# Kernel optimization log

Hardware: AMD Instinct MI355X
Metric: run time of the kernel (lower is better)

## Reference

```python
import jax, jax.numpy as jnp
import numpy as np

NB, C, N, H, W = 2, 128, 4, 64, 64
K = 9  # 3x3 kernel positions


def _conv(x, w, b, pad):
    y = jax.lax.conv_general_dilated(x, w, (1, 1), ((pad, pad), (pad, pad)),
                                     dimension_numbers=('NCHW', 'OIHW', 'NCHW'))
    return y + b[None, :, None, None]


def _bn(x, g, be, m, v, eps=1e-5):
    scale = g / jnp.sqrt(v + eps)
    return x * scale[None, :, None, None] + (be - m * scale)[None, :, None, None]


def _maxpool(x):
    # MaxPool2d(kernel_size=2, stride=1, padding=1): output H+1, W+1
    return jax.lax.reduce_window(x, -jnp.inf, jax.lax.max, (1, 1, 2, 2), (1, 1, 1, 1),
                                 ((0, 0), (0, 0), (1, 1), (1, 1)))


def _deform_conv(x, offset, mask, w, b):
    # modulated deformable conv v2, kernel 3x3, stride 1, padding 1
    n, c, h, wd = x.shape
    ky = jnp.repeat(jnp.arange(3), 3).astype(x.dtype)  # kernel row offsets
    kx = jnp.tile(jnp.arange(3), 3).astype(x.dtype)    # kernel col offsets
    dy = offset[:, 0::2]  # [n,K,h,w] (torchvision layout: interleaved dy,dx)
    dx = offset[:, 1::2]
    py = jnp.arange(h, dtype=x.dtype)[None, None, :, None] - 1.0 + ky[None, :, None, None] + dy
    px = jnp.arange(wd, dtype=x.dtype)[None, None, None, :] - 1.0 + kx[None, :, None, None] + dx
    y0 = jnp.floor(py)
    x0 = jnp.floor(px)
    wy = py - y0
    wx = px - x0
    xt = jnp.transpose(x, (0, 2, 3, 1))  # [n,h,w,c]
    bidx = jnp.arange(n)[:, None, None, None]

    def gather(yi, xi):
        valid = ((yi >= 0) & (yi < h) & (xi >= 0) & (xi < wd)).astype(x.dtype)
        yc = jnp.clip(yi, 0, h - 1).astype(jnp.int32)
        xc = jnp.clip(xi, 0, wd - 1).astype(jnp.int32)
        return xt[bidx, yc, xc] * valid[..., None]  # [n,K,h,w,c]

    v = (((1 - wy) * (1 - wx))[..., None] * gather(y0, x0)
         + ((1 - wy) * wx)[..., None] * gather(y0, x0 + 1)
         + (wy * (1 - wx))[..., None] * gather(y0 + 1, x0)
         + (wy * wx)[..., None] * gather(y0 + 1, x0 + 1))
    v = v * mask[..., None]  # modulation mask [n,K,h,w]
    out = jnp.einsum('nkhwc,ock->nohw', v, w.reshape(w.shape[0], c, K))
    return out + b[None, :, None, None]


def _forward(x, w1, b1, g1, be1, m1, v1, w_off, b_off, w_mod, b_mod, w_def, b_def,
             g2, be2, m2, v2, w_ds, b_ds, g3, be3, m3, v3):
    for i in range(NB):
        h = jax.nn.relu(_bn(_conv(x, w1[i], b1[i], 1), g1[i], be1[i], m1[i], v1[i]))
        off = _conv(h, w_off[i], b_off[i], 1)
        msk = 2.0 * jax.nn.sigmoid(_conv(h, w_mod[i], b_mod[i], 1))
        d = _bn(_deform_conv(h, off, msk, w_def[i], b_def[i]), g2[i], be2[i], m2[i], v2[i])
        res = _bn(_conv(x, w_ds[i], b_ds[i], 0), g3[i], be3[i], m3[i], v3[i])
        x = _maxpool(jax.nn.relu(d + res))
    return x


def setup_inputs() -> dict:
    key = jax.random.key(0)
    ks = iter(jax.random.split(key, 48))

    def rn(shape, s=0.05):
        return jax.random.normal(next(ks), shape, jnp.float32) * s

    def bnp():
        g = jax.random.uniform(next(ks), (NB, C), jnp.float32) * 0.5 + 0.75
        be = rn((NB, C), 0.1)
        m = rn((NB, C), 0.1)
        v = jax.random.uniform(next(ks), (NB, C), jnp.float32) * 0.5 + 0.75
        return g, be, m, v

    g1, be1, m1, v1 = bnp()
    g2, be2, m2, v2 = bnp()
    g3, be3, m3, v3 = bnp()
    return dict(
        x=jax.random.normal(next(ks), (N, C, H, W), jnp.float32),
        w1=rn((NB, C, C, 3, 3)), b1=rn((NB, C)),
        g1=g1, be1=be1, m1=m1, v1=v1,
        w_off=rn((NB, 2 * K, C, 3, 3), 0.01), b_off=rn((NB, 2 * K), 0.01),
        w_mod=rn((NB, K, C, 3, 3), 0.01), b_mod=rn((NB, K), 0.01),
        w_def=rn((NB, C, C, 3, 3)), b_def=rn((NB, C)),
        g2=g2, be2=be2, m2=m2, v2=v2,
        w_ds=rn((NB, C, C, 1, 1)), b_ds=rn((NB, C)),
        g3=g3, be3=be3, m3=m3, v3=v3,
    )


def reference(x, w1, b1, g1, be1, m1, v1, w_off, b_off, w_mod, b_mod, w_def, b_def,
              g2, be2, m2, v2, w_ds, b_ds, g3, be3, m3, v3):
    return _forward(x, w1, b1, g1, be1, m1, v1, w_off, b_off, w_mod, b_mod, w_def, b_def,
                    g2, be2, m2, v2, w_ds, b_ds, g3, be3, m3, v3)
```

## Files before the change

kernel.cpp:

```cpp
#include <hip/hip_runtime.h>
#include <math.h>

constexpr int NN = 4;
constexpr int CC = 128;

typedef unsigned short u16;
typedef short bfrag __attribute__((ext_vector_type(8)));
typedef float facc  __attribute__((ext_vector_type(4)));

__device__ __forceinline__ float bf2f(u16 v) {
    unsigned u = ((unsigned)v) << 16; float f; __builtin_memcpy(&f, &u, 4); return f;
}
__device__ __forceinline__ u16 f2bf(float f) {
    unsigned u; __builtin_memcpy(&u, &f, 4);
    unsigned r = u + 0x7FFFu + ((u >> 16) & 1u);
    return (u16)(r >> 16);
}

typedef const __attribute__((address_space(1))) unsigned int gu32;
typedef __attribute__((address_space(3))) unsigned int lu32;
__device__ __forceinline__ void gload16(const u16* g, u16* l) {
    __builtin_amdgcn_global_load_lds((gu32*)g, (lu32*)l, 16, 0, 0);
}

template<int WM, int WN, int MR, int NR, int NOB, int EPI>
__global__ __launch_bounds__(512)
void gconv_h(const u16* __restrict__ A, const u16* __restrict__ Wp,
             const float* __restrict__ bias, void* __restrict__ Out,
             int H, int W, int npb)
{
    constexpr int HALOW = 68;
    __shared__ __align__(16) u16 halo[4 * HALOW * 128];

    const int Hp = H + 2, Wq = W + 2, HW = H * W;
    const int tid = threadIdx.x, lane = tid & 63, wv = tid >> 6;
    const int wn = wv % WN, wm = wv / WN;
    const int colc = lane & 15, kg = lane >> 4;
    const int n = blockIdx.x / npb;
    const int pib = (blockIdx.x - n * npb) * 64;
    const int ymin = pib / W;

    {
        const u16* Abase = A + (size_t)n * Hp * Wq * 128;
        for (int c = wv; c < 4 * HALOW / 4; c += 8) {
            int o = c * 512 + lane * 8;
            int r = o / (HALOW * 128);
            int e = o - r * (HALOW * 128);
            int x = e >> 7;
            int g = (e >> 3) & 15;
            int xs = x < Wq ? x : Wq - 1;
            int pr = ymin + r; if (pr > Hp - 1) pr = Hp - 1;
            const u16* src = Abase + ((size_t)pr * Wq + xs) * 128 + (g ^ (x & 7)) * 8;
            gload16(src, &halo[c * 512]);
        }
    }
    __syncthreads();

    int dyr[MR], axr[MR];
#pragma unroll
    for (int r = 0; r < MR; ++r) {
        int m = wm * (MR * 16) + r * 16 + colc;
        int pixl = pib + m; if (pixl > HW - 1) pixl = HW - 1;
        int y = pixl / W;
        dyr[r] = y - ymin; axr[r] = pixl - y * W;
    }

    auto wfrag = [&](int tap, int cc, int q) -> const bfrag* {
        return (const bfrag*)(Wp + (size_t)tap * (NOB * 2048)
                              + ((cc * NOB + wn * NR + q) * 64 + lane) * 8);
    };

    bfrag bc[4][NR];
#pragma unroll
    for (int cc = 0; cc < 4; ++cc)
#pragma unroll
        for (int q = 0; q < NR; ++q) bc[cc][q] = *wfrag(0, cc, q);

    facc acc[MR][NR];
#pragma unroll
    for (int r = 0; r < MR; ++r)
#pragma unroll
        for (int q = 0; q < NR; ++q) acc[r][q] = (facc){0.f, 0.f, 0.f, 0.f};

#pragma unroll 1
    for (int t = 0; t < 9; ++t) {
        int ty = t / 3, tx = t - ty * 3;
        bfrag bn_[4][NR];
        if (t < 8) {
#pragma unroll
            for (int cc = 0; cc < 4; ++cc)
#pragma unroll
                for (int q = 0; q < NR; ++q) bn_[cc][q] = *wfrag(t + 1, cc, q);
        }
#pragma unroll
        for (int cc = 0; cc < 4; ++cc) {
            bfrag a[MR];
#pragma unroll
            for (int r = 0; r < MR; ++r) {
                int xx = axr[r] + tx;
                a[r] = *(const bfrag*)&halo[((dyr[r] + ty) * HALOW + xx) * 128
                                            + ((cc * 4 + kg) ^ (xx & 7)) * 8];
            }
#pragma unroll
            for (int r = 0; r < MR; ++r)
#pragma unroll
                for (int q = 0; q < NR; ++q)
                    acc[r][q] = __builtin_amdgcn_mfma_f32_16x16x32_bf16(a[r], bc[cc][q], acc[r][q], 0, 0, 0);
        }
        if (t < 8) {
#pragma unroll
            for (int cc = 0; cc < 4; ++cc)
#pragma unroll
                for (int q = 0; q < NR; ++q) bc[cc][q] = bn_[cc][q];
        }
    }

#pragma unroll
    for (int r = 0; r < MR; ++r) {
#pragma unroll
        for (int j = 0; j < 4; ++j) {
            int m = wm * (MR * 16) + r * 16 + kg * 4 + j;
            int pixl = pib + m;
            if (pixl >= HW) continue;
#pragma unroll
            for (int q = 0; q < NR; ++q) {
                int oc = wn * (NR * 16) + q * 16 + colc;
                float val = acc[r][q][j] + bias[oc];
                if constexpr (EPI == 0) {
                    val = fmaxf(val, 0.f);
                    int y = pixl / W, x = pixl - y * W;
                    ((u16*)Out)[((size_t)(n * Hp + y + 1) * Wq + x + 1) * 128 + oc] = f2bf(val);
                } else {
                    if (oc >= 18) val = 2.f / (1.f + expf(-val));
                    ((float*)Out)[((size_t)n * HW + pixl) * 32 + oc] = val;
                }
            }
        }
    }
}

__global__ __launch_bounds__(512, 4)
void deform2_k(const u16* __restrict__ Hb, const u16* __restrict__ Xp,
               const float* __restrict__ OM, const u16* __restrict__ Wp,
               const float* __restrict__ biasC, float* __restrict__ T,
               int H, int W, int tw, int th)
{
    __shared__ __align__(16) u16 halo[96 * 16 * 8];
    __shared__ __align__(16) float oml[32 * 32];
    __shared__ __align__(16) u16 As2[2][32 * 128];

    const int Hp = H + 2, Wq = W + 2, HW = H * W;
    const int tid = threadIdx.x, lane = tid & 63, wv = tid >> 6;
    const int wn = wv & 3, wm = wv >> 2;
    const int colc = lane & 15, kg = lane >> 4;
    int bt = blockIdx.x;
    int n = bt / (tw * th); int rt = bt - n * (tw * th);
    int ty0 = (rt / tw) * 4, tx0 = (rt - (rt / tw) * tw) * 8;
    const u16* Hbase = Hb + (size_t)n * Hp * Wq * 128;

#pragma unroll
    for (int c = 0; c < 3; ++c) {
        int g = c * 512 + tid;
        int s = g >> 4, u = g & 15;
        int row = s / 12, col = s - row * 12;
        int gy = min(max(ty0 - 2 + row, 0), H - 1);
        int gx = min(max(tx0 - 2 + col, 0), W - 1);
        int gr = u ^ (s & 15);
        gload16(Hbase + ((size_t)(gy + 1) * Wq + gx + 1) * 128 + gr * 8,
                &halo[(c * 512 + wv * 64) * 8]);
    }
    if (tid < 256) {
        int r = tid >> 3, q4 = tid & 7;
        int yy = min(ty0 + (r >> 3), H - 1), xx = min(tx0 + (r & 7), W - 1);
        gload16((const u16*)(OM + ((size_t)n * HW + yy * W + xx) * 32) + q4 * 8,
                (u16*)oml + wv * 64 * 8);
    }

    const int sg = tid & 15, srow = tid >> 4;
    const int sgz = sg ^ (srow & 7);
    const int cy = min(ty0 + (srow >> 3), H - 1), cx = min(tx0 + (srow & 7), W - 1);
    const size_t soffX = ((size_t)(n * Hp + cy + 1) * Wq + cx + 1) * 128 + sgz * 8;
    __syncthreads();

    auto sample = [&](int buf, int k) {
        int ky = k / 3, kx = k - ky * 3;
        float dy = oml[srow * 32 + 2 * k];
        float dx = oml[srow * 32 + 2 * k + 1];
        float mm = oml[srow * 32 + 18 + k];
        float pyf = (float)cy - 1.f + (float)ky + dy;
        float pxf = (float)cx - 1.f + (float)kx + dx;
        float fy = floorf(pyf), fx = floorf(pxf);
        int y0 = (int)fy, x0 = (int)fx;
        float wy = pyf - fy, wx = pxf - fx;
        bool y0v = (y0 >= 0) && (y0 < H), y1v = (y0 >= -1) && (y0 < H - 1);
        bool x0v = (x0 >= 0) && (x0 < W), x1v = (x0 >= -1) && (x0 < W - 1);
        int yc0 = min(max(y0, 0), H - 1), yc1 = min(max(y0 + 1, 0), H - 1);
        int xc0 = min(max(x0, 0), W - 1), xc1 = min(max(x0 + 1, 0), W - 1);
        float w00 = (1.f - wy) * (1.f - wx) * ((y0v && x0v) ? mm : 0.f);
        float w01 = (1.f - wy) * wx         * ((y0v && x1v) ? mm : 0.f);
        float w10 = wy * (1.f - wx)         * ((y1v && x0v) ? mm : 0.f);
        float w11 = wy * wx                 * ((y1v && x1v) ? mm : 0.f);
        int ry0 = yc0 - ty0 + 2, ry1 = yc1 - ty0 + 2;
        int rx0 = xc0 - tx0 + 2, rx1 = xc1 - tx0 + 2;
        bool allin = (unsigned)ry0 < 8u && (unsigned)ry1 < 8u
                  && (unsigned)rx0 < 12u && (unsigned)rx1 < 12u;
        bfrag c00, c01, c10, c11;
        if (allin) {
            int s00 = ry0 * 12 + rx0, s01 = ry0 * 12 + rx1;
            int s10 = ry1 * 12 + rx0, s11 = ry1 * 12 + rx1;
            c00 = *(const bfrag*)&halo[(s00 * 16 + (sg ^ (s00 & 15))) * 8];
            c01 = *(const bfrag*)&halo[(s01 * 16 + (sg ^ (s01 & 15))) * 8];
            c10 = *(const bfrag*)&halo[(s10 * 16 + (sg ^ (s10 & 15))) * 8];
            c11 = *(const bfrag*)&halo[(s11 * 16 + (sg ^ (s11 & 15))) * 8];
        } else {
            c00 = *(const bfrag*)(Hbase + ((size_t)(yc0 + 1) * Wq + xc0 + 1) * 128 + sg * 8);
            c01 = *(const bfrag*)(Hbase + ((size_t)(yc0 + 1) * Wq + xc1 + 1) * 128 + sg * 8);
            c10 = *(const bfrag*)(Hbase + ((size_t)(yc1 + 1) * Wq + xc0 + 1) * 128 + sg * 8);
            c11 = *(const bfrag*)(Hbase + ((size_t)(yc1 + 1) * Wq + xc1 + 1) * 128 + sg * 8);
        }
        bfrag o;
#pragma unroll
        for (int j = 0; j < 8; ++j) {
            float f = w00 * bf2f((u16)c00[j]) + w01 * bf2f((u16)c01[j])
                    + w10 * bf2f((u16)c10[j]) + w11 * bf2f((u16)c11[j]);
            o[j] = (short)f2bf(f);
        }
        *(bfrag*)&As2[buf][srow * 128 + sgz * 8] = o;
    };

    facc acc[2];
    acc[0] = (facc){0.f, 0.f, 0.f, 0.f};
    acc[1] = (facc){0.f, 0.f, 0.f, 0.f};

    sample(0, 0);
    __syncthreads();

#pragma unroll
    for (int t = 0; t < 10; ++t) {
        if (t < 8)       sample((t + 1) & 1, t + 1);
        else if (t == 8) gload16(Xp + soffX, &As2[1][wv * 512]);
        const u16* as = As2[t & 1];
        const int m = wm * 16 + colc;
#pragma unroll
        for (int cc = 0; cc < 4; ++cc) {
            bfrag a = *(const bfrag*)&as[m * 128 + ((cc * 4 + kg) ^ (m & 7)) * 8];
#pragma unroll
            for (int q = 0; q < 2; ++q) {
                bfrag b = *(const bfrag*)(Wp + (size_t)t * 16384
                            + ((cc * 8 + wn * 2 + q) * 64 + lane) * 8);
                acc[q] = __builtin_amdgcn_mfma_f32_16x16x32_bf16(a, b, acc[q], 0, 0, 0);
            }
        }
        __syncthreads();
    }

#pragma unroll
    for (int j = 0; j < 4; ++j) {
        int m = wm * 16 + kg * 4 + j;
        int y = ty0 + (m >> 3), x = tx0 + (m & 7);
        if (y >= H || x >= W) continue;
#pragma unroll
        for (int q = 0; q < 2; ++q) {
            int oc = wn * 32 + q * 16 + colc;
            T[((size_t)n * HW + y * W + x) * 128 + oc] = fmaxf(acc[q][j] + biasC[oc], 0.f);
        }
    }
}

template<int OUTMODE>
__global__ __launch_bounds__(256)
void pool_k(const float* __restrict__ T, void* __restrict__ Out, int H, int W)
{
    const int HW = H * W, Ho = H + 1, Wo = W + 1;
    int tot = NN * Ho * Wo * 16;
    int idx = blockIdx.x * 256 + threadIdx.x;
    if (idx >= tot) return;
    int cg = idx & 15; int t = idx >> 4;
    int ox = t % Wo; t /= Wo; int oy = t % Ho; int n = t / Ho;

    float mx[8];
#pragma unroll
    for (int j = 0; j < 8; ++j) mx[j] = -INFINITY;
#pragma unroll
    for (int d = 0; d < 2; ++d) {
        int iy = oy - 1 + d;
        if (iy < 0 || iy >= H) continue;
#pragma unroll
        for (int e = 0; e < 2; ++e) {
            int ix = ox - 1 + e;
            if (ix < 0 || ix >= W) continue;
            const float* src = T + ((size_t)(n * HW + iy * W + ix)) * 128 + cg * 8;
#pragma unroll
            for (int j = 0; j < 8; ++j) mx[j] = fmaxf(mx[j], src[j]);
        }
    }
    if constexpr (OUTMODE == 0) {
        int Hp2 = Ho + 2, Wp2 = Wo + 2;
        bfrag o;
#pragma unroll
        for (int j = 0; j < 8; ++j) o[j] = (short)f2bf(mx[j]);
        *(bfrag*)((u16*)Out + ((size_t)(n * Hp2 + oy + 1) * Wp2 + (ox + 1)) * 128 + cg * 8) = o;
    } else {
#pragma unroll
        for (int j = 0; j < 8; ++j) {
            int c = cg * 8 + j;
            ((float*)Out)[(((size_t)n * 128 + c) * Ho + oy) * Wo + ox] = mx[j];
        }
    }
}

__global__ __launch_bounds__(256)
void prep_k(u16* __restrict__ Xp0, u16* __restrict__ Xp1,
            u16* __restrict__ Hp0, u16* __restrict__ Hp1)
{
    const int G0 = (NN * 66 * 66 * 128) / 8;
    const int G1 = (NN * 67 * 67 * 128) / 8;
    int idx = blockIdx.x * 256 + threadIdx.x;
    bfrag z = (bfrag){0, 0, 0, 0, 0, 0, 0, 0};
    if (idx < G0) { *(bfrag*)(Xp0 + (size_t)idx * 8) = z; return; }
    idx -= G0;
    if (idx < G1) { *(bfrag*)(Xp1 + (size_t)idx * 8) = z; return; }
    idx -= G1;
    if (idx < G0) { *(bfrag*)(Hp0 + (size_t)idx * 8) = z; return; }
    idx -= G0;
    if (idx < G1) { *(bfrag*)(Hp1 + (size_t)idx * 8) = z; return; }
}

__global__ __launch_bounds__(256)
void x0_to_nhwc(const float* __restrict__ x0, u16* __restrict__ Xp)
{
    int idx = blockIdx.x * 256 + threadIdx.x;
    if (idx >= NN * 64 * 64 * 16) return;
    int cg = idx & 15; int t = idx >> 4;
    int x = t & 63; t >>= 6; int y = t & 63; int n = t >> 6;
    bfrag o;
#pragma unroll
    for (int j = 0; j < 8; ++j) {
        int c = cg * 8 + j;
        o[j] = (short)f2bf(x0[(((size_t)n * 128 + c) * 64 + y) * 64 + x]);
    }
    *(bfrag*)(Xp + ((size_t)(n * 66 + y + 1) * 66 + (x + 1)) * 128 + cg * 8) = o;
}

__global__ __launch_bounds__(256)
void wprep_k(const float* __restrict__ w1, const float* __restrict__ b1,
             const float* __restrict__ g1, const float* __restrict__ be1,
             const float* __restrict__ m1, const float* __restrict__ v1,
             const float* __restrict__ w_off, const float* __restrict__ b_off,
             const float* __restrict__ w_mod, const float* __restrict__ b_mod,
             const float* __restrict__ w_def, const float* __restrict__ b_def,
             const float* __restrict__ g2, const float* __restrict__ be2,
             const float* __restrict__ m2, const float* __restrict__ v2,
             const float* __restrict__ w_ds, const float* __restrict__ b_ds,
             const float* __restrict__ g3, const float* __restrict__ be3,
             const float* __restrict__ m3, const float* __restrict__ v3,
             u16* __restrict__ Wb1p, u16* __restrict__ Wbomp, u16* __restrict__ Wbdp,
             float* __restrict__ bias1f, float* __restrict__ biasOM, float* __restrict__ biasC)
{
    const int C1 = 9 * 4 * 8 * 512;
    const int C2 = 9 * 4 * 2 * 512;
    const int C3 = 10 * 4 * 8 * 512;
    int idx = blockIdx.x * 256 + threadIdx.x;
    if (idx < 2 * C1) {
        int inst = idx / C1, e = idx - inst * C1;
        int j = e & 7, lane = (e >> 3) & 63, rest = e >> 9;
        int ob = rest & 7; rest >>= 3; int cc = rest & 3; int tap = rest >> 2;
        int oc = ob * 16 + (lane & 15), c = cc * 32 + (lane >> 4) * 8 + j;
        float sc = g1[inst * 128 + oc] * rsqrtf(v1[inst * 128 + oc] + 1e-5f);
        Wb1p[idx] = f2bf(sc * w1[(((size_t)inst * 128 + oc) * 128 + c) * 9 + tap]);
        return;
    }
    idx -= 2 * C1;
    if (idx < 2 * C2) {
        int inst = idx / C2, e = idx - inst * C2;
        int j = e & 7, lane = (e >> 3) & 63, rest = e >> 9;
        int ob = rest & 1; rest >>= 1; int cc = rest & 3; int tap = rest >> 2;
        int oc = ob * 16 + (lane & 15), c = cc * 32 + (lane >> 4) * 8 + j;
        float v = 0.f;
        if (oc < 18)      v = w_off[(((size_t)inst * 18 + oc) * 128 + c) * 9 + tap];
        else if (oc < 27) v = w_mod[(((size_t)inst * 9 + (oc - 18)) * 128 + c) * 9 + tap];
        Wbomp[inst * C2 + e] = f2bf(v);
        return;
    }
    idx -= 2 * C2;
    if (idx < 2 * C3) {
        int inst = idx / C3, e = idx - inst * C3;
        int j = e & 7, lane = (e >> 3) & 63, rest = e >> 9;
        int ob = rest & 7; rest >>= 3; int cc = rest & 3; int tap = rest >> 2;
        int oc = ob * 16 + (lane & 15), c = cc * 32 + (lane >> 4) * 8 + j;
        float val;
        if (tap < 9) {
            float sc2 = g2[inst * 128 + oc] * rsqrtf(v2[inst * 128 + oc] + 1e-5f);
            val = sc2 * w_def[(((size_t)inst * 128 + oc) * 128 + c) * 9 + tap];
        } else {
            float sc3 = g3[inst * 128 + oc] * rsqrtf(v3[inst * 128 + oc] + 1e-5f);
            val = sc3 * w_ds[((size_t)inst * 128 + oc) * 128 + c];
        }
        Wbdp[inst * C3 + e] = f2bf(val);
        return;
    }
    idx -= 2 * C3;
    if (idx < 2 * 288) {
        int inst = idx / 288, r = idx - inst * 288;
        if (r < 128) {
            int oc = r, o = inst * 128 + oc;
            float sc = g1[o] * rsqrtf(v1[o] + 1e-5f);
            bias1f[o] = sc * b1[o] + be1[o] - m1[o] * sc;
        } else if (r < 160) {
            int oc = r - 128;
            float v = 0.f;
            if (oc < 18)      v = b_off[inst * 18 + oc];
            else if (oc < 27) v = b_mod[inst * 9 + (oc - 18)];
            biasOM[inst * 32 + oc] = v;
        } else {
            int oc = r - 160, o = inst * 128 + oc;
            float sc2 = g2[o] * rsqrtf(v2[o] + 1e-5f);
            float sc3 = g3[o] * rsqrtf(v3[o] + 1e-5f);
            biasC[o] = sc2 * b_def[o] + (be2[o] - m2[o] * sc2)
                     + sc3 * b_ds[o] + (be3[o] - m3[o] * sc3);
        }
    }
}

extern "C" void kernel_launch(void* const* d_in, const int* in_sizes, int n_in,
                              void* d_out, int out_size, void* d_ws, size_t ws_size,
                              hipStream_t stream)
{
    const float* x0    = (const float*)d_in[0];
    const float* w1    = (const float*)d_in[1];
    const float* b1    = (const float*)d_in[2];
    const float* g1    = (const float*)d_in[3];
    const float* be1   = (const float*)d_in[4];
    const float* m1    = (const float*)d_in[5];
    const float* v1    = (const float*)d_in[6];
    const float* w_off = (const float*)d_in[7];
    const float* b_off = (const float*)d_in[8];
    const float* w_mod = (const float*)d_in[9];
    const float* b_mod = (const float*)d_in[10];
    const float* w_def = (const float*)d_in[11];
    const float* b_def = (const float*)d_in[12];
    const float* g2    = (const float*)d_in[13];
    const float* be2   = (const float*)d_in[14];
    const float* m2    = (const float*)d_in[15];
    const float* v2    = (const float*)d_in[16];
    const float* w_ds  = (const float*)d_in[17];
    const float* b_ds  = (const float*)d_in[18];
    const float* g3    = (const float*)d_in[19];
    const float* be3   = (const float*)d_in[20];
    const float* m3    = (const float*)d_in[21];
    const float* v3    = (const float*)d_in[22];

    const int C1 = 147456, C2 = 36864, C3 = 163840;
    char* wsp = (char*)d_ws;
    auto alloc = [&](size_t bytes) { char* r = wsp; wsp += (bytes + 255) & ~(size_t)255; return r; };
    const size_t szX0 = (size_t)NN * 66 * 66 * 128 * 2;
    const size_t szX1 = (size_t)NN * 67 * 67 * 128 * 2;
    u16*   Xpad0  = (u16*)alloc(szX0);
    u16*   Xpad1  = (u16*)alloc(szX1);
    u16*   Hpad0  = (u16*)alloc(szX0);
    u16*   Hpad1  = (u16*)alloc(szX1);
    float* OFFMSK = (float*)alloc((size_t)16900 * 32 * 4);
    float* T      = (float*)alloc((size_t)16900 * 128 * 4);
    u16*   Wb1p   = (u16*)alloc((size_t)2 * C1 * 2);
    u16*   Wbomp  = (u16*)alloc((size_t)2 * C2 * 2);
    u16*   Wbdp   = (u16*)alloc((size_t)2 * C3 * 2);
    float* bias1f = (float*)alloc(2 * 128 * 4);
    float* biasOM = (float*)alloc(2 * 32 * 4);
    float* biasC  = (float*)alloc(2 * 128 * 4);

    const int G0 = (NN * 66 * 66 * 128) / 8, G1 = (NN * 67 * 67 * 128) / 8;
    int ztot = 2 * G0 + 2 * G1;
    prep_k<<<(ztot + 255) / 256, 256, 0, stream>>>(Xpad0, Xpad1, Hpad0, Hpad1);
    x0_to_nhwc<<<(NN * 64 * 64 * 16 + 255) / 256, 256, 0, stream>>>(x0, Xpad0);
    int ptot = 2 * C1 + 2 * C2 + 2 * C3 + 2 * 288;
    wprep_k<<<(ptot + 255) / 256, 256, 0, stream>>>(
        w1, b1, g1, be1, m1, v1, w_off, b_off, w_mod, b_mod, w_def, b_def,
        g2, be2, m2, v2, w_ds, b_ds, g3, be3, m3, v3,
        Wb1p, Wbomp, Wbdp, bias1f, biasOM, biasC);

    const u16* curX = Xpad0;
    for (int i = 0; i < 2; ++i) {
        int H = 64 + i, W = 64 + i;
        int HW = H * W;
        int npb = (HW + 63) / 64;
        int grid = NN * npb;
        u16* Hpad = (i == 0) ? Hpad0 : Hpad1;

        gconv_h<2, 4, 2, 2, 8, 0><<<grid, 512, 0, stream>>>(
            curX, Wb1p + (size_t)i * C1, bias1f + i * 128, Hpad, H, W, npb);
        gconv_h<4, 2, 1, 1, 2, 1><<<grid, 512, 0, stream>>>(
            Hpad, Wbomp + (size_t)i * C2, biasOM + i * 32, OFFMSK, H, W, npb);
        int tw = (W + 7) / 8, th = (H + 3) / 4;
        deform2_k<<<NN * tw * th, 512, 0, stream>>>(
            Hpad, curX, OFFMSK, Wbdp + (size_t)i * C3, biasC + i * 128, T, H, W, tw, th);
        if (i == 0) {
            pool_k<0><<<(NN * 65 * 65 * 16 + 255) / 256, 256, 0, stream>>>(T, Xpad1, H, W);
        } else {
            pool_k<1><<<(NN * 66 * 66 * 16 + 255) / 256, 256, 0, stream>>>(T, d_out, H, W);
        }
        curX = Xpad1;
    }
}
```

Measured before the change: 139.1 us.

## Sample deformable inputs directly into MFMA A-fragments, removing LDS staging and barriers

The deform kernel now lets each lane bilinearly sample exactly the A-operand fragment it feeds to the MFMA, so the double-buffered As2 LDS staging and the per-tap __syncthreads are gone. The offset/mask tile is loaded into LDS transposed so per-pixel reads are contiguous, and all weight fragments for a tap are loaded before the MFMAs. In exchange, each pixel's sampling is repeated across the four wn warps (4x redundant bilinear math and halo reads), and register pressure rises.

```diff
diff --git a/kernel.cpp b/kernel.cpp
--- a/kernel.cpp
+++ b/kernel.cpp
@@ -140,14 +140,13 @@
 }
 
 __global__ __launch_bounds__(512, 4)
-void deform2_k(const u16* __restrict__ Hb, const u16* __restrict__ Xp,
+void deform3_k(const u16* __restrict__ Hb, const u16* __restrict__ Xp,
                const float* __restrict__ OM, const u16* __restrict__ Wp,
                const float* __restrict__ biasC, float* __restrict__ T,
                int H, int W, int tw, int th)
 {
     __shared__ __align__(16) u16 halo[96 * 16 * 8];
-    __shared__ __align__(16) float oml[32 * 32];
-    __shared__ __align__(16) u16 As2[2][32 * 128];
+    __shared__ __align__(16) float oml[27 * 32];
 
     const int Hp = H + 2, Wq = W + 2, HW = H * W;
     const int tid = threadIdx.x, lane = tid & 63, wv = tid >> 6;
@@ -169,95 +168,96 @@
         gload16(Hbase + ((size_t)(gy + 1) * Wq + gx + 1) * 128 + gr * 8,
                 &halo[(c * 512 + wv * 64) * 8]);
     }
-    if (tid < 256) {
-        int r = tid >> 3, q4 = tid & 7;
-        int yy = min(ty0 + (r >> 3), H - 1), xx = min(tx0 + (r & 7), W - 1);
-        gload16((const u16*)(OM + ((size_t)n * HW + yy * W + xx) * 32) + q4 * 8,
-                (u16*)oml + wv * 64 * 8);
-    }
-
-    const int sg = tid & 15, srow = tid >> 4;
-    const int sgz = sg ^ (srow & 7);
-    const int cy = min(ty0 + (srow >> 3), H - 1), cx = min(tx0 + (srow & 7), W - 1);
-    const size_t soffX = ((size_t)(n * Hp + cy + 1) * Wq + cx + 1) * 128 + sgz * 8;
+    for (int e = tid; e < 27 * 32; e += 512) {
+        int f = e >> 5, m2 = e & 31;
+        int yy = min(ty0 + (m2 >> 3), H - 1), xx = min(tx0 + (m2 & 7), W - 1);
+        oml[e] = OM[((size_t)n * HW + yy * W + xx) * 32 + f];
+    }
     __syncthreads();
 
-    auto sample = [&](int buf, int k) {
-        int ky = k / 3, kx = k - ky * 3;
-        float dy = oml[srow * 32 + 2 * k];
-        float dx = oml[srow * 32 + 2 * k + 1];
-        float mm = oml[srow * 32 + 18 + k];
-        float pyf = (float)cy - 1.f + (float)ky + dy;
-        float pxf = (float)cx - 1.f + (float)kx + dx;
-        float fy = floorf(pyf), fx = floorf(pxf);
-        int y0 = (int)fy, x0 = (int)fx;
-        float wy = pyf - fy, wx = pxf - fx;
-        bool y0v = (y0 >= 0) && (y0 < H), y1v = (y0 >= -1) && (y0 < H - 1);
-        bool x0v = (x0 >= 0) && (x0 < W), x1v = (x0 >= -1) && (x0 < W - 1);
-        int yc0 = min(max(y0, 0), H - 1), yc1 = min(max(y0 + 1, 0), H - 1);
-        int xc0 = min(max(x0, 0), W - 1), xc1 = min(max(x0 + 1, 0), W - 1);
-        float w00 = (1.f - wy) * (1.f - wx) * ((y0v && x0v) ? mm : 0.f);
-        float w01 = (1.f - wy) * wx         * ((y0v && x1v) ? mm : 0.f);
-        float w10 = wy * (1.f - wx)         * ((y1v && x0v) ? mm : 0.f);
-        float w11 = wy * wx                 * ((y1v && x1v) ? mm : 0.f);
-        int ry0 = yc0 - ty0 + 2, ry1 = yc1 - ty0 + 2;
-        int rx0 = xc0 - tx0 + 2, rx1 = xc1 - tx0 + 2;
-        bool allin = (unsigned)ry0 < 8u && (unsigned)ry1 < 8u
-                  && (unsigned)rx0 < 12u && (unsigned)rx1 < 12u;
-        bfrag c00, c01, c10, c11;
-        if (allin) {
-            int s00 = ry0 * 12 + rx0, s01 = ry0 * 12 + rx1;
-            int s10 = ry1 * 12 + rx0, s11 = ry1 * 12 + rx1;
-            c00 = *(const bfrag*)&halo[(s00 * 16 + (sg ^ (s00 & 15))) * 8];
-            c01 = *(const bfrag*)&halo[(s01 * 16 + (sg ^ (s01 & 15))) * 8];
-            c10 = *(const bfrag*)&halo[(s10 * 16 + (sg ^ (s10 & 15))) * 8];
-            c11 = *(const bfrag*)&halo[(s11 * 16 + (sg ^ (s11 & 15))) * 8];
-        } else {
-            c00 = *(const bfrag*)(Hbase + ((size_t)(yc0 + 1) * Wq + xc0 + 1) * 128 + sg * 8);
-            c01 = *(const bfrag*)(Hbase + ((size_t)(yc0 + 1) * Wq + xc1 + 1) * 128 + sg * 8);
-            c10 = *(const bfrag*)(Hbase + ((size_t)(yc1 + 1) * Wq + xc0 + 1) * 128 + sg * 8);
-            c11 = *(const bfrag*)(Hbase + ((size_t)(yc1 + 1) * Wq + xc1 + 1) * 128 + sg * 8);
-        }
-        bfrag o;
-#pragma unroll
-        for (int j = 0; j < 8; ++j) {
-            float f = w00 * bf2f((u16)c00[j]) + w01 * bf2f((u16)c01[j])
-                    + w10 * bf2f((u16)c10[j]) + w11 * bf2f((u16)c11[j]);
-            o[j] = (short)f2bf(f);
-        }
-        *(bfrag*)&As2[buf][srow * 128 + sgz * 8] = o;
-    };
+    const int m = wm * 16 + colc;
+    const int upy = ty0 + (m >> 3), upx = tx0 + (m & 7);
+    const int cy = min(upy, H - 1), cx = min(upx, W - 1);
+    const size_t xoff = ((size_t)(n * Hp + cy + 1) * Wq + cx + 1) * 128;
 
     facc acc[2];
     acc[0] = (facc){0.f, 0.f, 0.f, 0.f};
     acc[1] = (facc){0.f, 0.f, 0.f, 0.f};
 
-    sample(0, 0);
-    __syncthreads();
-
 #pragma unroll
     for (int t = 0; t < 10; ++t) {
-        if (t < 8)       sample((t + 1) & 1, t + 1);
-        else if (t == 8) gload16(Xp + soffX, &As2[1][wv * 512]);
-        const u16* as = As2[t & 1];
-        const int m = wm * 16 + colc;
-#pragma unroll
-        for (int cc = 0; cc < 4; ++cc) {
-            bfrag a = *(const bfrag*)&as[m * 128 + ((cc * 4 + kg) ^ (m & 7)) * 8];
-#pragma unroll
-            for (int q = 0; q < 2; ++q) {
-                bfrag b = *(const bfrag*)(Wp + (size_t)t * 16384
+        bfrag b[4][2];
+#pragma unroll
+        for (int cc = 0; cc < 4; ++cc)
+#pragma unroll
+            for (int q = 0; q < 2; ++q)
+                b[cc][q] = *(const bfrag*)(Wp + (size_t)t * 16384
                             + ((cc * 8 + wn * 2 + q) * 64 + lane) * 8);
-                acc[q] = __builtin_amdgcn_mfma_f32_16x16x32_bf16(a, b, acc[q], 0, 0, 0);
+
+        bfrag a[4];
+        if (t < 9) {
+            float dy = oml[(2 * t) * 32 + m];
+            float dx = oml[(2 * t + 1) * 32 + m];
+            float mm = oml[(18 + t) * 32 + m];
+            float pyf = (float)cy - 1.f + (float)(t / 3) + dy;
+            float pxf = (float)cx - 1.f + (float)(t % 3) + dx;
+            float fy = floorf(pyf), fx = floorf(pxf);
+            int y0 = (int)fy, x0 = (int)fx;
+            float wy = pyf - fy, wx = pxf - fx;
+            bool y0v = (y0 >= 0) && (y0 < H), y1v = (y0 >= -1) && (y0 < H - 1);
+            bool x0v = (x0 >= 0) && (x0 < W), x1v = (x0 >= -1) && (x0 < W - 1);
+            int yc0 = min(max(y0, 0), H - 1), yc1 = min(max(y0 + 1, 0), H - 1);
+            int xc0 = min(max(x0, 0), W - 1), xc1 = min(max(x0 + 1, 0), W - 1);
+            float w00 = (1.f - wy) * (1.f - wx) * ((y0v && x0v) ? mm : 0.f);
+            float w01 = (1.f - wy) * wx         * ((y0v && x1v) ? mm : 0.f);
+            float w10 = wy * (1.f - wx)         * ((y1v && x0v) ? mm : 0.f);
+            float w11 = wy * wx                 * ((y1v && x1v) ? mm : 0.f);
+            int ry0 = yc0 - ty0 + 2, ry1 = yc1 - ty0 + 2;
+            int rx0 = xc0 - tx0 + 2, rx1 = xc1 - tx0 + 2;
+            bool allin = (unsigned)ry0 < 8u && (unsigned)ry1 < 8u
+                      && (unsigned)rx0 < 12u && (unsigned)rx1 < 12u;
+            int s00 = ry0 * 12 + rx0, s01 = ry0 * 12 + rx1;
+            int s10 = ry1 * 12 + rx0, s11 = ry1 * 12 + rx1;
+#pragma unroll
+            for (int cc = 0; cc < 4; ++cc) {
+                int g = cc * 4 + kg;
+                bfrag c00, c01, c10, c11;
+                if (allin) {
+                    c00 = *(const bfrag*)&halo[(s00 * 16 + (g ^ (s00 & 15))) * 8];
+                    c01 = *(const bfrag*)&halo[(s01 * 16 + (g ^ (s01 & 15))) * 8];
+                    c10 = *(const bfrag*)&halo[(s10 * 16 + (g ^ (s10 & 15))) * 8];
+                    c11 = *(const bfrag*)&halo[(s11 * 16 + (g ^ (s11 & 15))) * 8];
+                } else {
+                    c00 = *(const bfrag*)(Hbase + ((size_t)(yc0 + 1) * Wq + xc0 + 1) * 128 + g * 8);
+                    c01 = *(const bfrag*)(Hbase + ((size_t)(yc0 + 1) * Wq + xc1 + 1) * 128 + g * 8);
+                    c10 = *(const bfrag*)(Hbase + ((size_t)(yc1 + 1) * Wq + xc0 + 1) * 128 + g * 8);
+                    c11 = *(const bfrag*)(Hbase + ((size_t)(yc1 + 1) * Wq + xc1 + 1) * 128 + g * 8);
+                }
+                bfrag o;
+#pragma unroll
+                for (int j = 0; j < 8; ++j) {
+                    float f = w00 * bf2f((u16)c00[j]) + w01 * bf2f((u16)c01[j])
+                            + w10 * bf2f((u16)c10[j]) + w11 * bf2f((u16)c11[j]);
+                    o[j] = (short)f2bf(f);
+                }
+                a[cc] = o;
             }
-        }
-        __syncthreads();
+        } else {
+#pragma unroll
+            for (int cc = 0; cc < 4; ++cc)
+                a[cc] = *(const bfrag*)(Xp + xoff + (cc * 4 + kg) * 8);
+        }
+#pragma unroll
+        for (int cc = 0; cc < 4; ++cc)
+#pragma unroll
+            for (int q = 0; q < 2; ++q)
+                acc[q] = __builtin_amdgcn_mfma_f32_16x16x32_bf16(a[cc], b[cc][q], acc[q], 0, 0, 0);
     }
 
 #pragma unroll
     for (int j = 0; j < 4; ++j) {
-        int m = wm * 16 + kg * 4 + j;
-        int y = ty0 + (m >> 3), x = tx0 + (m & 7);
+        int md = wm * 16 + kg * 4 + j;
+        int y = ty0 + (md >> 3), x = tx0 + (md & 7);
         if (y >= H || x >= W) continue;
 #pragma unroll
         for (int q = 0; q < 2; ++q) {
@@ -491,7 +491,7 @@
         gconv_h<4, 2, 1, 1, 2, 1><<<grid, 512, 0, stream>>>(
             Hpad, Wbomp + (size_t)i * C2, biasOM + i * 32, OFFMSK, H, W, npb);
         int tw = (W + 7) / 8, th = (H + 3) / 4;
-        deform2_k<<<NN * tw * th, 512, 0, stream>>>(
+        deform3_k<<<NN * tw * th, 512, 0, stream>>>(
             Hpad, curX, OFFMSK, Wbdp + (size_t)i * C3, biasC + i * 128, T, H, W, tw, th);
         if (i == 0) {
             pool_k<0><<<(NN * 65 * 65 * 16 + 255) / 256, 256, 0, stream>>>(T, Xpad1, H, W);
```

Result: slower. 214.0 us (+53.9%).
